# Performance work log

Hardware: AMD Instinct MI355X
Metric: run time of the kernel (lower is better)

## Reference

```python
import jax, jax.numpy as jnp
import numpy as np

NEG_SLOPE = 0.01  # torch nn.LeakyReLU default

B, N, IN_F, OUT_F, HEADS = 4, 2048, 512, 512, 8
D = OUT_F // HEADS  # 64


def setup_inputs() -> dict:
    key = jax.random.key(0)
    ks = jax.random.split(key, 4)
    X = jax.random.normal(ks[0], (B, N, IN_F), dtype=jnp.float32)
    W_v = jax.random.normal(ks[1], (IN_F, D), dtype=jnp.float32) * (IN_F ** -0.5)
    b_v = jnp.zeros((D,), dtype=jnp.float32)
    W_q = jax.random.normal(ks[2], (D, HEADS), dtype=jnp.float32) * (D ** -0.5)
    b_q = jnp.zeros((HEADS,), dtype=jnp.float32)
    W_k = jax.random.normal(ks[3], (D, HEADS), dtype=jnp.float32) * (D ** -0.5)
    b_k = jnp.zeros((HEADS,), dtype=jnp.float32)
    return {"X": X, "W_v": W_v, "b_v": b_v, "W_q": W_q, "b_q": b_q, "W_k": W_k, "b_k": b_k}


def reference(X, W_v, b_v, W_q, b_q, W_k, b_k):
    # V: (B, N, D)
    V = X @ W_v + b_v
    # per-node, per-head scalar scores: (B, N, H) -> (B, H, N)
    Q = jnp.swapaxes(V @ W_q + b_q, 1, 2)
    K = jnp.swapaxes(V @ W_k + b_k, 1, 2)
    # A[b,h,i,j] = leaky_relu(Q[b,h,j] + K[b,h,i])  (broadcast outer-sum)
    A = jax.nn.leaky_relu(Q[:, :, None, :] + K[:, :, :, None], negative_slope=NEG_SLOPE)
    A = jax.nn.softmax(A, axis=-1)  # dropout = identity in eval mode
    # H[b,i,h,f] = sum_j A[b,h,i,j] V[b,j,f]
    H = jnp.einsum('bhij,bjf->bihf', A, V)
    return H.reshape(H.shape[0], H.shape[1], -1)  # (B, N, H*D)
```

## Files before the change

kernel.cpp:

```cpp
#include <hip/hip_runtime.h>

#define BB   4
#define NN   2048
#define INF  512
#define HH   8
#define DD   64
#define BH   (BB*HH)
#define NCK  16
#define CKS  128


__global__ __launch_bounds__(256) void k_vq(
    const float* __restrict__ X, const float* __restrict__ Wv,
    const float* __restrict__ bv,
    const float* __restrict__ Wq, const float* __restrict__ bq,
    const float* __restrict__ Wk, const float* __restrict__ bk,
    float* __restrict__ V, float* __restrict__ ksg,
    unsigned long long* __restrict__ qk64)
{
  __shared__ float Ws[4][64][68];
  __shared__ float red[3][32][64];
  __shared__ float Vs[32][65];
  const int t  = threadIdx.x;
  const int kh = t >> 6;
  const int u  = t & 63;
  const int tc = u & 15;
  const int rw = u >> 4;
  const int r0 = blockIdx.x * 32;
  float acc[8][4];
  #pragma unroll
  for (int r = 0; r < 8; r++)
    #pragma unroll
    for (int c = 0; c < 4; c++) acc[r][c] = 0.f;

  for (int kc = 0; kc < 128; kc += 64) {
    __syncthreads();
    #pragma unroll
    for (int i = 0; i < 16; i++) {
      const int e4 = u + i * 64;
      const int k  = e4 >> 4;
      const int n4 = (e4 & 15) * 4;
      *(float4*)(&Ws[kh][k][n4]) =
          *(const float4*)(Wv + (size_t)(kh * 128 + kc + k) * DD + n4);
    }
    __syncthreads();
    const float* xp = X + (size_t)(r0 + rw * 8) * INF + kh * 128 + kc;
    #pragma unroll 2
    for (int kk = 0; kk < 64; kk += 4) {
      float4 xr[8];
      #pragma unroll
      for (int r = 0; r < 8; r++)
        xr[r] = *(const float4*)(xp + (size_t)r * INF + kk);
      #pragma unroll
      for (int j = 0; j < 4; j++) {
        const float4 w4 = *(const float4*)(&Ws[kh][kk + j][tc * 4]);
        #pragma unroll
        for (int r = 0; r < 8; r++) {
          const float x = (j == 0) ? xr[r].x : (j == 1) ? xr[r].y
                        : (j == 2) ? xr[r].z : xr[r].w;
          acc[r][0] += x * w4.x;  acc[r][1] += x * w4.y;
          acc[r][2] += x * w4.z;  acc[r][3] += x * w4.w;
        }
      }
    }
  }

  __syncthreads();
  if (kh > 0) {
    #pragma unroll
    for (int r = 0; r < 8; r++)
      #pragma unroll
      for (int c = 0; c < 4; c++)
        red[kh - 1][r * 4 + c][u] = acc[r][c];
  }
  __syncthreads();
  if (kh == 0) {
    const float4 bb = *(const float4*)(bv + tc * 4);
    #pragma unroll
    for (int r = 0; r < 8; r++) {
      float4 o;
      o.x = acc[r][0] + red[0][r*4+0][u] + red[1][r*4+0][u] + red[2][r*4+0][u] + bb.x;
      o.y = acc[r][1] + red[0][r*4+1][u] + red[1][r*4+1][u] + red[2][r*4+1][u] + bb.y;
      o.z = acc[r][2] + red[0][r*4+2][u] + red[1][r*4+2][u] + red[2][r*4+2][u] + bb.z;
      o.w = acc[r][3] + red[0][r*4+3][u] + red[1][r*4+3][u] + red[2][r*4+3][u] + bb.w;
      *(float4*)(V + (size_t)(r0 + rw * 8 + r) * DD + tc * 4) = o;
      Vs[rw * 8 + r][tc * 4]     = o.x;  Vs[rw * 8 + r][tc * 4 + 1] = o.y;
      Vs[rw * 8 + r][tc * 4 + 2] = o.z;  Vs[rw * 8 + r][tc * 4 + 3] = o.w;
    }
  }
  __syncthreads();

  const int row = t >> 3;
  const int h   = t & 7;
  float sq = bq[h], sk = bk[h];
  #pragma unroll 8
  for (int dd = 0; dd < DD; dd++) {
    const float v = Vs[row][dd];
    sq += v * Wq[dd * HH + h];
    sk += v * Wk[dd * HH + h];
  }
  const int grow = r0 + row;
  const int b = grow >> 11, n = grow & (NN - 1);
  const int bh = b * HH + h;
  ksg[bh * NN + n] = sk;
  unsigned uo = __float_as_uint(sq);
  uo = (uo & 0x80000000u) ? ~uo : (uo | 0x80000000u);
  qk64[(size_t)bh * NN + n] = ((unsigned long long)uo << 32) | (unsigned)n;
}

__global__ __launch_bounds__(256) void k_rank(
    const unsigned long long* __restrict__ qk64,
    float* __restrict__ sqs, unsigned short* __restrict__ idxg)
{
  __shared__ __align__(16) unsigned long long keys[NN];
  __shared__ int cnt[8][256];
  const int t    = threadIdx.x;
  const int bh   = blockIdx.x >> 3;
  const int slab = blockIdx.x & 7;
  const int jq   = t & 31;
  const int kq   = t >> 5;
  const unsigned long long* __restrict__ kb = qk64 + (size_t)bh * NN;

  {
    const ulonglong2* __restrict__ g2 = (const ulonglong2*)kb;
    ulonglong2* s2 = (ulonglong2*)keys;
    #pragma unroll
    for (int x = 0; x < 4; x++) s2[t + 256 * x] = g2[t + 256 * x];
  }
  __syncthreads();

  const int jg = (slab << 8) | (jq << 3);
  unsigned long long kj[8];
  #pragma unroll
  for (int u2 = 0; u2 < 8; u2++) kj[u2] = keys[jg + u2];

  int c[8] = {0, 0, 0, 0, 0, 0, 0, 0};
  const ulonglong2* __restrict__ k2 = (const ulonglong2*)(keys + kq * 256);
  #pragma unroll 8
  for (int l = 0; l < 128; l++) {
    const ulonglong2 kk = k2[l];
    #pragma unroll
    for (int u2 = 0; u2 < 8; u2++)
      c[u2] += (kk.x < kj[u2]) + (kk.y < kj[u2]);
  }
  #pragma unroll
  for (int u2 = 0; u2 < 8; u2++) cnt[kq][u2 * 32 + jq] = c[u2];
  __syncthreads();

  {
    const int jl = t;
    const int ci = (jl & 7) * 32 + (jl >> 3);
    int rank = 0;
    #pragma unroll
    for (int q = 0; q < 8; q++) rank += cnt[q][ci];
    const unsigned long long kj2 = keys[(slab << 8) | jl];
    const unsigned uo = (unsigned)(kj2 >> 32);
    const unsigned ur = (uo & 0x80000000u) ? (uo & 0x7fffffffu) : ~uo;
    sqs [bh * NN + rank] = __uint_as_float(ur);
    idxg[bh * NN + rank] = (unsigned short)((slab << 8) | jl);
  }
}

__global__ __launch_bounds__(256) void k_csum(
    const float* __restrict__ sqs, const unsigned short* __restrict__ idxg,
    const float* __restrict__ V,
    float* __restrict__ S1g, float* __restrict__ S2g,
    float* __restrict__ SL1, float* __restrict__ SL2)
{
  __shared__ float ss1[4][64], ss2[4][64];
  __shared__ float sl1[4], sl2[4];
  const int t  = threadIdx.x;
  const int bh = blockIdx.x >> 4;
  const int ck = blockIdx.x & 15;
  const int d  = t & 63, g = t >> 6;
  const int r0 = ck * CKS + g * 32;
  const float* Vb  = V + (size_t)(bh >> 3) * NN * DD;
  const float* sqb = sqs + bh * NN;
  const unsigned short* ib = idxg + bh * NN;
  float a1 = 0.f, a2 = 0.f, s1 = 0.f, s2 = 0.f;
  #pragma unroll 8
  for (int rr = 0; rr < 32; rr++) {
    const int r = r0 + rr;
    const float qv = sqb[r];
    const float e1 = __expf(qv), e2 = __expf(0.01f * qv);
    const float v  = Vb[(size_t)ib[r] * DD + d];
    a1 += e1 * v;  a2 += e2 * v;  s1 += e1;  s2 += e2;
  }
  ss1[g][d] = a1;  ss2[g][d] = a2;
  if (d == 0) { sl1[g] = s1;  sl2[g] = s2; }
  __syncthreads();
  if (g == 0) {
    S1g[(bh*NCK + ck)*64 + d] = ss1[0][d]+ss1[1][d]+ss1[2][d]+ss1[3][d];
    S2g[(bh*NCK + ck)*64 + d] = ss2[0][d]+ss2[1][d]+ss2[2][d]+ss2[3][d];
    if (d == 0) {
      SL1[bh*NCK + ck] = sl1[0]+sl1[1]+sl1[2]+sl1[3];
      SL2[bh*NCK + ck] = sl2[0]+sl2[1]+sl2[2]+sl2[3];
    }
  }
}

__global__ __launch_bounds__(256) void k_out2(
    const float* __restrict__ sqs, const unsigned short* __restrict__ idxg,
    const float* __restrict__ V, const float* __restrict__ ksg,
    const float* __restrict__ S1g, const float* __restrict__ S2g,
    const float* __restrict__ SL1, const float* __restrict__ SL2,
    float* __restrict__ out)
{
  __shared__ float P1l[CKS + 1][64];
  __shared__ float P2l[CKS + 1][64];
  __shared__ float sqc[CKS];
  __shared__ float Ll1[CKS + 1], Ll2[CKS + 1];
  __shared__ __align__(16) unsigned char scr[12304];
  __shared__ int nwl;

  float (*ss1)[64] = (float(*)[64])scr;
  float (*ss2)[64] = (float(*)[64])(scr + 1024);
  float* sl1 = (float*)(scr + 2048);
  float* sl2 = (float*)(scr + 2064);
  unsigned short* wl = (unsigned short*)scr;
  float* kwl = (float*)(scr + 4096);

  const int t  = threadIdx.x;
  const int bh = blockIdx.x >> 4;
  const int ck = blockIdx.x & 15;
  const int d  = t & 63, g = t >> 6;
  const int r0 = ck * CKS + g * 32;
  const int b  = bh >> 3, h = bh & 7;
  const float* Vb  = V + (size_t)b * NN * DD;
  const float* sqb = sqs + bh * NN;
  const unsigned short* ib = idxg + bh * NN;

  if (t < CKS) sqc[t] = sqb[ck * CKS + t];
  if (t == 0) nwl = 0;

  float a1 = 0.f, a2 = 0.f, s1 = 0.f, s2 = 0.f;
  #pragma unroll 8
  for (int rr = 0; rr < 32; rr++) {
    const int r = r0 + rr;
    const float qv = sqb[r];
    const float e1 = __expf(qv), e2 = __expf(0.01f * qv);
    const float v  = Vb[(size_t)ib[r] * DD + d];
    P1l[g * 32 + rr][d] = v;
    a1 += e1 * v;  a2 += e2 * v;  s1 += e1;  s2 += e2;
  }
  ss1[g][d] = a1;  ss2[g][d] = a2;
  if (d == 0) { sl1[g] = s1;  sl2[g] = s2; }
  __syncthreads();
  float o1 = 0.f, o2 = 0.f, lo1 = 0.f, lo2 = 0.f;
  for (int gg = 0; gg < g; gg++) { o1 += ss1[gg][d]; o2 += ss2[gg][d]; lo1 += sl1[gg]; lo2 += sl2[gg]; }

  a1 = o1;  a2 = o2;  s1 = lo1;  s2 = lo2;
  #pragma unroll 8
  for (int rr = 0; rr < 32; rr++) {
    const int row = g * 32 + rr;
    const float qv = sqb[r0 + rr];
    const float e1 = __expf(qv), e2 = __expf(0.01f * qv);
    const float v  = P1l[row][d];
    P1l[row][d] = a1;
    P2l[row][d] = a2;
    if (d == 0) { Ll1[row] = s1;  Ll2[row] = s2; }
    a1 += e1 * v;  a2 += e2 * v;  s1 += e1;  s2 += e2;
  }
  if (g == 3) {
    P1l[CKS][d] = a1;  P2l[CKS][d] = a2;
    if (d == 0) { Ll1[CKS] = s1;  Ll2[CKS] = s2; }
  }
  __syncthreads();

  float of1 = 0.f, of2 = 0.f, t1 = 0.f, t2 = 0.f;
  float so1 = 0.f, so2 = 0.f, lt1 = 0.f, lt2 = 0.f;
  #pragma unroll
  for (int c2 = 0; c2 < NCK; c2++) {
    const float v1 = S1g[(bh*NCK + c2)*64 + d];
    const float v2 = S2g[(bh*NCK + c2)*64 + d];
    const float w1 = SL1[bh*NCK + c2];
    const float w2 = SL2[bh*NCK + c2];
    t1 += v1;  t2 += v2;  lt1 += w1;  lt2 += w2;
    if (c2 < ck) { of1 += v1; of2 += v2; so1 += w1; so2 += w2; }
  }
  const float qlo = ck ? sqb[ck * CKS - 1] : -__builtin_inff();
  const float qhi = (ck < NCK - 1) ? sqc[CKS - 1] : __builtin_inff();

  const float* kb = ksg + bh * NN;
  #pragma unroll
  for (int s = 0; s < 8; s++) {
    const int i = t + 256 * s;
    const float kv = kb[i];
    const float tt = -kv;
    if (qlo <= tt && tt < qhi) {
      const int slot = atomicAdd(&nwl, 1);
      wl[slot]  = (unsigned short)i;
      kwl[slot] = kv;
    }
  }
  __syncthreads();

  const float sq0 = sqc[d];
  const float sq1 = sqc[64 + d];
  const int n = nwl;
  for (int e = g; e < n; e += 4) {
    const int i = wl[e];
    const float kv = kwl[e];
    const float tt = -kv;
    const unsigned long long b0 = __ballot(sq0 <= tt);
    const unsigned long long b1 = __ballot(sq1 <= tt);
    const int loc = __popcll(b0) + __popcll(b1);
    const float p1v = of1 + P1l[loc][d];
    const float p2v = of2 + P2l[loc][d];
    const float q1v = so1 + Ll1[loc];
    const float q2v = so2 + Ll2[loc];
    const float ek  = __expf(kv);
    const float ek2 = __expf(0.01f * kv);
    const float num = ek * (t1  - p1v) + ek2 * p2v;
    const float den = ek * (lt1 - q1v) + ek2 * q2v;
    out[((size_t)(b * NN + i)) * (HH * DD) + h * DD + d] = num / den;
  }
}

extern "C" void kernel_launch(void* const* d_in, const int* in_sizes, int n_in,
                              void* d_out, int out_size, void* d_ws, size_t ws_size,
                              hipStream_t stream)
{
  (void)in_sizes; (void)n_in; (void)out_size; (void)ws_size;
  const float* X  = (const float*)d_in[0];
  const float* Wv = (const float*)d_in[1];
  const float* bv = (const float*)d_in[2];
  const float* Wq = (const float*)d_in[3];
  const float* bq = (const float*)d_in[4];
  const float* Wk = (const float*)d_in[5];
  const float* bk = (const float*)d_in[6];
  float* out = (float*)d_out;

  float* w = (float*)d_ws;
  float* V     = w;  w += (size_t)BB*NN*DD;
  float* ksg   = w;  w += BH*NN;
  unsigned short* idxg = (unsigned short*)w;  w += BH*NN/2;
  float* S1g   = w;  w += (size_t)BH*NCK*DD;
  float* S2g   = w;  w += (size_t)BH*NCK*DD;
  float* SL1   = w;  w += BH*NCK;
  float* SL2   = w;  w += BH*NCK;
  float* sqs   = w;  w += BH*NN;
  unsigned long long* qk64 = (unsigned long long*)w;  w += BH*NN*2;

  k_vq   <<<256, 256, 0, stream>>>(X, Wv, bv, Wq, bq, Wk, bk, V, ksg, qk64);
  k_rank <<<BH*8, 256, 0, stream>>>(qk64, sqs, idxg);
  k_csum <<<BH*NCK, 256, 0, stream>>>(sqs, idxg, V, S1g, S2g, SL1, SL2);
  k_out2 <<<BH*NCK, 256, 0, stream>>>(sqs, idxg, V, ksg, S1g, S2g, SL1, SL2, out);
}
```

Measured before the change: 131.8 us.

## Fuse chunk-sum computation into rank kernel via per-slab partial sums

Removes the separate k_csum kernel. Each rank block now buckets its 256 nodes by sorted chunk and accumulates exp-weighted V partial sums per chunk, slab-locally with coalesced V rows. k_out2 then reduces the 8 slab partials per chunk. This saves one launch and the gather pass over sorted indices, at the cost of extra partial-sum storage, more reads in k_out2, and more work in k_rank.

```diff
diff --git a/kernel.cpp b/kernel.cpp
--- a/kernel.cpp
+++ b/kernel.cpp
@@ -110,10 +110,15 @@
 
 __global__ __launch_bounds__(256) void k_rank(
     const unsigned long long* __restrict__ qk64,
-    float* __restrict__ sqs, unsigned short* __restrict__ idxg)
+    const float* __restrict__ V,
+    float* __restrict__ sqs, unsigned short* __restrict__ idxg,
+    float* __restrict__ PS1, float* __restrict__ PS2,
+    float* __restrict__ PL1, float* __restrict__ PL2)
 {
   __shared__ __align__(16) unsigned long long keys[NN];
   __shared__ int cnt[8][256];
+  __shared__ unsigned short mlist[NCK][CKS];
+  __shared__ int mcnt[NCK];
   const int t    = threadIdx.x;
   const int bh   = blockIdx.x >> 3;
   const int slab = blockIdx.x & 7;
@@ -121,6 +126,7 @@
   const int kq   = t >> 5;
   const unsigned long long* __restrict__ kb = qk64 + (size_t)bh * NN;
 
+  if (t < NCK) mcnt[t] = 0;
   {
     const ulonglong2* __restrict__ g2 = (const ulonglong2*)kb;
     ulonglong2* s2 = (ulonglong2*)keys;
@@ -158,52 +164,61 @@
     const unsigned ur = (uo & 0x80000000u) ? (uo & 0x7fffffffu) : ~uo;
     sqs [bh * NN + rank] = __uint_as_float(ur);
     idxg[bh * NN + rank] = (unsigned short)((slab << 8) | jl);
-  }
-}
-
-__global__ __launch_bounds__(256) void k_csum(
-    const float* __restrict__ sqs, const unsigned short* __restrict__ idxg,
-    const float* __restrict__ V,
-    float* __restrict__ S1g, float* __restrict__ S2g,
-    float* __restrict__ SL1, float* __restrict__ SL2)
-{
-  __shared__ float ss1[4][64], ss2[4][64];
-  __shared__ float sl1[4], sl2[4];
-  const int t  = threadIdx.x;
-  const int bh = blockIdx.x >> 4;
-  const int ck = blockIdx.x & 15;
-  const int d  = t & 63, g = t >> 6;
-  const int r0 = ck * CKS + g * 32;
-  const float* Vb  = V + (size_t)(bh >> 3) * NN * DD;
-  const float* sqb = sqs + bh * NN;
-  const unsigned short* ib = idxg + bh * NN;
-  float a1 = 0.f, a2 = 0.f, s1 = 0.f, s2 = 0.f;
-  #pragma unroll 8
-  for (int rr = 0; rr < 32; rr++) {
-    const int r = r0 + rr;
-    const float qv = sqb[r];
-    const float e1 = __expf(qv), e2 = __expf(0.01f * qv);
-    const float v  = Vb[(size_t)ib[r] * DD + d];
-    a1 += e1 * v;  a2 += e2 * v;  s1 += e1;  s2 += e2;
-  }
-  ss1[g][d] = a1;  ss2[g][d] = a2;
-  if (d == 0) { sl1[g] = s1;  sl2[g] = s2; }
-  __syncthreads();
-  if (g == 0) {
-    S1g[(bh*NCK + ck)*64 + d] = ss1[0][d]+ss1[1][d]+ss1[2][d]+ss1[3][d];
-    S2g[(bh*NCK + ck)*64 + d] = ss2[0][d]+ss2[1][d]+ss2[2][d]+ss2[3][d];
-    if (d == 0) {
-      SL1[bh*NCK + ck] = sl1[0]+sl1[1]+sl1[2]+sl1[3];
-      SL2[bh*NCK + ck] = sl2[0]+sl2[1]+sl2[2]+sl2[3];
-    }
+    const int ck  = rank >> 7;
+    const int pos = atomicAdd(&mcnt[ck], 1);
+    mlist[ck][pos] = (unsigned short)jl;
+  }
+  __syncthreads();
+
+  const float* Vb = V + (size_t)(bh >> 3) * NN * DD;
+  const int d = t & 63;
+  const int w = t >> 6;
+  #pragma unroll
+  for (int cc = 0; cc < 4; cc++) {
+    const int ck = w + cc * 4;
+    const int m  = mcnt[ck];
+    float a1 = 0.f, a2 = 0.f, s1 = 0.f, s2 = 0.f;
+    for (int e0 = 0; e0 < CKS; e0 += 16) {
+      if (e0 >= m) break;
+      int lj[16];
+      #pragma unroll
+      for (int x = 0; x < 16; x++) {
+        const int e = e0 + x;
+        lj[x] = mlist[ck][(e < m) ? e : 0];
+      }
+      float w1[16], w2[16];
+      #pragma unroll
+      for (int x = 0; x < 16; x++) {
+        const unsigned long long kk = keys[(slab << 8) | lj[x]];
+        const unsigned o2 = (unsigned)(kk >> 32);
+        const unsigned r2 = (o2 & 0x80000000u) ? (o2 & 0x7fffffffu) : ~o2;
+        const float q = __uint_as_float(r2);
+        w1[x] = __expf(q);  w2[x] = __expf(0.01f * q);
+      }
+      float v[16];
+      #pragma unroll
+      for (int x = 0; x < 16; x++)
+        v[x] = Vb[(size_t)((slab << 8) | lj[x]) * DD + d];
+      #pragma unroll
+      for (int x = 0; x < 16; x++) {
+        if (e0 + x < m) {
+          a1 += w1[x] * v[x];  a2 += w2[x] * v[x];
+          s1 += w1[x];         s2 += w2[x];
+        }
+      }
+    }
+    const size_t pb = (size_t)(bh * 8 + slab) * NCK + ck;
+    PS1[pb * 64 + d] = a1;
+    PS2[pb * 64 + d] = a2;
+    if (d == 0) { PL1[pb] = s1;  PL2[pb] = s2; }
   }
 }
 
 __global__ __launch_bounds__(256) void k_out2(
     const float* __restrict__ sqs, const unsigned short* __restrict__ idxg,
     const float* __restrict__ V, const float* __restrict__ ksg,
-    const float* __restrict__ S1g, const float* __restrict__ S2g,
-    const float* __restrict__ SL1, const float* __restrict__ SL2,
+    const float* __restrict__ PS1, const float* __restrict__ PS2,
+    const float* __restrict__ PL1, const float* __restrict__ PL2,
     float* __restrict__ out)
 {
   __shared__ float P1l[CKS + 1][64];
@@ -269,12 +284,16 @@
 
   float of1 = 0.f, of2 = 0.f, t1 = 0.f, t2 = 0.f;
   float so1 = 0.f, so2 = 0.f, lt1 = 0.f, lt2 = 0.f;
-  #pragma unroll
   for (int c2 = 0; c2 < NCK; c2++) {
-    const float v1 = S1g[(bh*NCK + c2)*64 + d];
-    const float v2 = S2g[(bh*NCK + c2)*64 + d];
-    const float w1 = SL1[bh*NCK + c2];
-    const float w2 = SL2[bh*NCK + c2];
+    float v1 = 0.f, v2 = 0.f, w1 = 0.f, w2 = 0.f;
+    #pragma unroll
+    for (int s = 0; s < 8; s++) {
+      const size_t pb = (size_t)(bh * 8 + s) * NCK + c2;
+      v1 += PS1[pb * 64 + d];
+      v2 += PS2[pb * 64 + d];
+      w1 += PL1[pb];
+      w2 += PL2[pb];
+    }
     t1 += v1;  t2 += v2;  lt1 += w1;  lt2 += w2;
     if (c2 < ck) { of1 += v1; of2 += v2; so1 += w1; so2 += w2; }
   }
@@ -335,15 +354,14 @@
   float* V     = w;  w += (size_t)BB*NN*DD;
   float* ksg   = w;  w += BH*NN;
   unsigned short* idxg = (unsigned short*)w;  w += BH*NN/2;
-  float* S1g   = w;  w += (size_t)BH*NCK*DD;
-  float* S2g   = w;  w += (size_t)BH*NCK*DD;
-  float* SL1   = w;  w += BH*NCK;
-  float* SL2   = w;  w += BH*NCK;
+  float* PS1   = w;  w += (size_t)BH*8*NCK*DD;
+  float* PS2   = w;  w += (size_t)BH*8*NCK*DD;
+  float* PL1   = w;  w += BH*8*NCK;
+  float* PL2   = w;  w += BH*8*NCK;
   float* sqs   = w;  w += BH*NN;
   unsigned long long* qk64 = (unsigned long long*)w;  w += BH*NN*2;
 
   k_vq   <<<256, 256, 0, stream>>>(X, Wv, bv, Wq, bq, Wk, bk, V, ksg, qk64);
-  k_rank <<<BH*8, 256, 0, stream>>>(qk64, sqs, idxg);
-  k_csum <<<BH*NCK, 256, 0, stream>>>(sqs, idxg, V, S1g, S2g, SL1, SL2);
-  k_out2 <<<BH*NCK, 256, 0, stream>>>(sqs, idxg, V, ksg, S1g, S2g, SL1, SL2, out);
+  k_rank <<<BH*8, 256, 0, stream>>>(qk64, V, sqs, idxg, PS1, PS2, PL1, PL2);
+  k_out2 <<<BH*NCK, 256, 0, stream>>>(sqs, idxg, V, ksg, PS1, PS2, PL1, PL2, out);
 }
```

Result: slower. 143.5 us (+8.9%).
